# Performance work log

Hardware: AMD Instinct MI355X
Metric: run time of the kernel (lower is better)

## Reference

```python
import jax, jax.numpy as jnp
import numpy as np

B, T, K, H = 2, 2048, 1024, 16


def setup_inputs() -> dict:
    key = jax.random.key(0)
    ks = jax.random.split(key, 9)
    sc = 0.02
    return {
        "x": jax.random.normal(ks[0], (B, T, K), dtype=jnp.float32),
        "Wq_w": jax.random.normal(ks[1], (K, K), dtype=jnp.float32) * sc,
        "Wq_b": jax.random.normal(ks[2], (K,), dtype=jnp.float32) * sc,
        "Wk_w": jax.random.normal(ks[3], (K, K), dtype=jnp.float32) * sc,
        "Wk_b": jax.random.normal(ks[4], (K,), dtype=jnp.float32) * sc,
        "Wv_w": jax.random.normal(ks[5], (K, K), dtype=jnp.float32) * sc,
        "Wv_b": jax.random.normal(ks[6], (K,), dtype=jnp.float32) * sc,
        "Wo_w": jax.random.normal(ks[7], (K, K), dtype=jnp.float32) * sc,
        "Wo_b": jax.random.normal(ks[8], (K,), dtype=jnp.float32) * sc,
    }


def reference(x, Wq_w, Wq_b, Wk_w, Wk_b, Wv_w, Wv_b, Wo_w, Wo_b):
    b, t, k = x.shape
    h = H
    s = k // h
    # nn.Linear: y = x @ W^T + b
    q = x @ Wq_w.T + Wq_b
    kk = x @ Wk_w.T + Wk_b
    v = x @ Wv_w.T + Wv_b
    # [b, t, h, s] -> [b, h, t, s]
    q = q.reshape(b, t, h, s).transpose(0, 2, 1, 3)
    kk = kk.reshape(b, t, h, s).transpose(0, 2, 1, 3)
    v = v.reshape(b, t, h, s).transpose(0, 2, 1, 3)
    # scores [b, h, t, t]
    dot = jnp.einsum("bhqd,bhkd->bhqk", q, kk)
    # causal mask: upper triangle (offset=1) set to -inf BEFORE scaling
    causal = jnp.tril(jnp.ones((t, t), dtype=bool))
    dot = jnp.where(causal, dot, -jnp.inf)
    # NOTE: original scales by sqrt(k) (full model dim), not sqrt(head_dim)
    dot = dot / jnp.sqrt(jnp.asarray(k, dot.dtype))
    attn = jax.nn.softmax(dot, axis=-1)
    out = jnp.einsum("bhqk,bhkd->bhqd", attn, v)  # [b, h, t, s]
    out = out.transpose(0, 2, 1, 3).reshape(b, t, k)
    return out @ Wo_w.T + Wo_b
```

## Files before the change

### kernel.cpp

```cpp
#include <hip/hip_runtime.h>

typedef unsigned short u16;
typedef unsigned int u32;
typedef __bf16 bf16x8 __attribute__((ext_vector_type(8)));
typedef float f32x4 __attribute__((ext_vector_type(4)));
typedef unsigned short u16x8 __attribute__((ext_vector_type(8)));
typedef unsigned int u32x4 __attribute__((ext_vector_type(4)));

#define B_ 2
#define T_ 2048
#define K_ 1024
#define H_ 16
#define S_ 64
#define MKC 4194304
#define QSCALE 0.04508422f

__device__ __forceinline__ u16 f2bf(float f) {
  unsigned int u = __builtin_bit_cast(unsigned int, f);
  u += 0x7fffu + ((u >> 16) & 1u);
  return (u16)(u >> 16);
}

__device__ __forceinline__ f32x4 MFMA(bf16x8 a, bf16x8 b, f32x4 c) {
  return __builtin_amdgcn_mfma_f32_16x16x32_bf16(a, b, c, 0, 0, 0);
}

__device__ __forceinline__ void gld16(const void* g, void* l) {
  __builtin_amdgcn_global_load_lds((const __attribute__((address_space(1))) void*)g,
                                   (__attribute__((address_space(3))) void*)l, 16, 0, 0);
}

template <int N>
__device__ __forceinline__ void waitv() {
  asm volatile("s_waitcnt vmcnt(%0)" ::"i"(N) : "memory");
}
__device__ __forceinline__ void memfence_barrier() {
  asm volatile("" ::: "memory");
  __builtin_amdgcn_s_barrier();
}

__global__ __launch_bounds__(256) void cvt_all(const float* __restrict__ x,
                                               const float* __restrict__ W0,
                                               const float* __restrict__ W1,
                                               const float* __restrict__ W2,
                                               const float* __restrict__ W3,
                                               u16* __restrict__ xb,
                                               u16* __restrict__ wb) {
  const int i = blockIdx.x * 256 + threadIdx.x;
  const float* src;
  u16* dst;
  if (i < 524288) {
    src = x + (size_t)i * 8;
    dst = xb + (size_t)i * 8;
  } else {
    const int j = i - 524288;
    const int sel = j >> 17;
    const float* W = sel == 0 ? W0 : sel == 1 ? W1 : sel == 2 ? W2 : W3;
    src = W + (size_t)(j & 131071) * 8;
    dst = wb + (size_t)j * 8;
  }
  const float4* s = (const float4*)src;
  float4 f0 = s[0], f1 = s[1];
  u16x8 p;
  p[0] = f2bf(f0.x); p[1] = f2bf(f0.y); p[2] = f2bf(f0.z); p[3] = f2bf(f0.w);
  p[4] = f2bf(f1.x); p[5] = f2bf(f1.y); p[6] = f2bf(f1.z); p[7] = f2bf(f1.w);
  *(u16x8*)dst = p;
}

template <int OMODE, int BN>
__global__ __launch_bounds__(256) void gemm16(const u16* __restrict__ A,
                                              const u16* __restrict__ Bm,
                                              const float* __restrict__ b0,
                                              const float* __restrict__ b1,
                                              const float* __restrict__ b2,
                                              void* __restrict__ C0,
                                              int M, int N, int K) {
  constexpr int NF = BN / 32;
  constexpr int SOPS = 2 + BN / 64;
  __shared__ u16 As[2][128 * 32];
  __shared__ u16 Bs[2][BN * 32];
  const int bm = blockIdx.x * 128;
  const int bn = blockIdx.y * BN;
  const int tid = threadIdx.x;
  const int w = tid >> 6, lane = tid & 63;
  const int wr = (w >> 1) * 64, wc = (w & 1) * (BN / 2);
  const int lr = lane & 15, g = lane >> 4;
  const int lk = g * 8;
  const int srow = lane >> 2, scol = (lane & 3) * 8;

  f32x4 acc[4][NF] = {};

  auto stg = [&](int buf, int k0) {
#pragma unroll
    for (int i = 0; i < 2; ++i) {
      const int rbase = (i * 4 + w) * 16;
      gld16(A + (size_t)(bm + rbase + srow) * K + k0 + scol, &As[buf][rbase * 32]);
    }
#pragma unroll
    for (int i = 0; i < BN / 64; ++i) {
      const int rbase = (i * 4 + w) * 16;
      gld16(Bm + (size_t)(bn + rbase + srow) * K + k0 + scol, &Bs[buf][rbase * 32]);
    }
  };

  stg(0, 0);
  const int NK = K >> 5;
  for (int kk = 0; kk < NK; ++kk) {
    const int buf = kk & 1;
    const bool pf = (kk + 1 < NK);
    if (pf) {
      stg(buf ^ 1, (kk + 1) * 32);
      waitv<SOPS>();
    } else {
      waitv<0>();
    }
    __builtin_amdgcn_s_barrier();
    bf16x8 af[4], bfr[NF];
#pragma unroll
    for (int m = 0; m < 4; ++m)
      af[m] = *(const bf16x8*)&As[buf][(wr + m * 16 + lr) * 32 + lk];
#pragma unroll
    for (int n = 0; n < NF; ++n)
      bfr[n] = *(const bf16x8*)&Bs[buf][(wc + n * 16 + lr) * 32 + lk];
#pragma unroll
    for (int m = 0; m < 4; ++m)
#pragma unroll
      for (int n = 0; n < NF; ++n)
        acc[m][n] = MFMA(af[m], bfr[n], acc[m][n]);
    memfence_barrier();
  }

  const int sel = (OMODE == 2) ? 0 : (bn >> 10);
  const float* bp = (OMODE == 2) ? b0 : (sel == 0 ? b0 : sel == 1 ? b1 : b2);
#pragma unroll
  for (int n = 0; n < NF; ++n) {
    const int col = bn + wc + n * 16 + lr;
    const float bv = bp[(OMODE == 2) ? col : (col & 1023)];
#pragma unroll
    for (int m = 0; m < 4; ++m) {
#pragma unroll
      for (int r = 0; r < 4; ++r) {
        const int row = bm + wr + m * 16 + g * 4 + r;
        float v = acc[m][n][r] + bv;
        if (OMODE == 2) {
          ((float*)C0)[(size_t)row * N + col] = v;
        } else {
          u16* dst = (u16*)C0;
          const int cc = col & 1023;
          if (sel == 2) {
            const int bb = row >> 11, t = row & 2047, hh = cc >> 6, ss = cc & 63;
            dst[(size_t)2 * MKC + (((size_t)(bb * H_ + hh) * S_ + ss) << 11) + t] = f2bf(v);
          } else {
            if (sel == 0) v *= QSCALE;
            dst[(size_t)sel * MKC + (size_t)row * 1024 + cc] = f2bf(v);
          }
        }
      }
    }
  }
}

__global__ __launch_bounds__(256) void attn_fwd(const u16* __restrict__ Q,
                                                const u16* __restrict__ Kb,
                                                const u16* __restrict__ Vt,
                                                u16* __restrict__ O) {
  __shared__ u16 Ks[2][64 * 64];
  __shared__ u16 Vs[2][64 * 64];
  const int tid = threadIdx.x;
  const int w = tid >> 6, lane = tid & 63;
  const int qh = lane & 15;
  const int g = lane >> 4;
  const int bh = blockIdx.x;
  const int b = bh >> 4, h = bh & 15;
  const int yy = blockIdx.y, t7 = yy & 7, kq = yy >> 3;
  const int qtile = (kq == 0) ? (31 - t7) : (kq == 1) ? (16 + t7)
                   : (kq == 2) ? (15 - t7) : t7;
  const int qb = qtile * 64;
  const int qw = qb + w * 16;
  const int myq = qw + qh;

  const size_t qoff = (size_t)(b * T_ + qw + qh) * K_ + h * S_ + g * 8;
  const bf16x8 bq0 = *(const bf16x8*)(Q + qoff);
  const bf16x8 bq1 = *(const bf16x8*)(Q + qoff + 32);

  const int srow = lane >> 3;
  const int sl8 = ((lane & 7) ^ srow) * 8;
  int kvp[2];
#pragma unroll
  for (int i = 0; i < 2; ++i) {
    const int rho = w * 16 + i * 8 + srow;
    const int a = rho >> 4;
    kvp[i] = ((a >> 1) << 5) | (((rho >> 2) & 3) << 3) | ((a & 1) << 2) | (rho & 3);
  }
  auto stage = [&](int buf, int k0) {
#pragma unroll
    for (int i = 0; i < 2; ++i) {
      const int rb = w * 16 + i * 8;
      gld16(Kb + (size_t)(b * T_ + k0 + kvp[i]) * K_ + h * S_ + sl8,
            &Ks[buf][rb * 64]);
    }
#pragma unroll
    for (int i = 0; i < 2; ++i) {
      const int rb = w * 16 + i * 8;
      gld16(Vt + (size_t)(bh * S_ + rb + srow) * T_ + k0 + sl8,
            &Vs[buf][rb * 64]);
    }
  };

  const int nk = qtile + 1;
  stage(0, 0);

  float m = -INFINITY, lsum = 0.f;
  f32x4 o[4] = {};
  const int ksw = qh & 7;

  for (int kt = 0; kt < nk; ++kt) {
    const int k0 = kt * 64;
    const int cur = kt & 1;
    const bool pf = (kt + 1 < nk);
    if (pf) {
      stage(cur ^ 1, k0 + 64);
      waitv<4>();
    } else {
      waitv<0>();
    }
    __builtin_amdgcn_s_barrier();

    f32x4 s[4];
    __builtin_amdgcn_s_setprio(1);
#pragma unroll
    for (int a = 0; a < 4; ++a) {
      const u16* kr = &Ks[cur][(a * 16 + qh) * 64];
      const bf16x8 kf0 = *(const bf16x8*)(kr + ((g ^ ksw) * 8));
      const bf16x8 kf1 = *(const bf16x8*)(kr + (((4 + g) ^ ksw) * 8));
      f32x4 z = {0.f, 0.f, 0.f, 0.f};
      z = MFMA(kf0, bq0, z);
      s[a] = MFMA(kf1, bq1, z);
    }
    __builtin_amdgcn_s_setprio(0);

    float p[4][4];
    float vmax = -INFINITY;
    if (k0 + 63 > qw) {
#pragma unroll
      for (int a = 0; a < 4; ++a)
#pragma unroll
        for (int r = 0; r < 4; ++r) {
          const int kv = k0 + ((a >> 1) << 5) + (g << 3) + ((a & 1) << 2) + r;
          p[a][r] = (kv <= myq) ? s[a][r] : -INFINITY;
          vmax = fmaxf(vmax, p[a][r]);
        }
    } else {
#pragma unroll
      for (int a = 0; a < 4; ++a)
#pragma unroll
        for (int r = 0; r < 4; ++r) {
          p[a][r] = s[a][r];
          vmax = fmaxf(vmax, p[a][r]);
        }
    }
    vmax = fmaxf(vmax, __shfl_xor(vmax, 16));
    vmax = fmaxf(vmax, __shfl_xor(vmax, 32));

    if (__any(vmax > m + 11.5f)) {
      const float mnew = fmaxf(m, vmax);
      const float alpha = __builtin_amdgcn_exp2f(m - mnew);
      m = mnew;
      lsum *= alpha;
      float aR[4];
#pragma unroll
      for (int r = 0; r < 4; ++r) aR[r] = __shfl(alpha, 4 * g + r);
#pragma unroll
      for (int n = 0; n < 4; ++n)
#pragma unroll
        for (int r = 0; r < 4; ++r) o[n][r] *= aR[r];
    }

    float ls = 0.f;
#pragma unroll
    for (int a = 0; a < 4; ++a)
#pragma unroll
      for (int r = 0; r < 4; ++r) {
        p[a][r] = __builtin_amdgcn_exp2f(p[a][r] - m);
        ls += p[a][r];
      }
    ls += __shfl_xor(ls, 16);
    ls += __shfl_xor(ls, 32);
    lsum += ls;

    __builtin_amdgcn_s_setprio(1);
#pragma unroll
    for (int c = 0; c < 2; ++c) {
      u32 t0, t1, t2, t3;
      asm("v_cvt_pk_bf16_f32 %0, %1, %2" : "=v"(t0) : "v"(p[2 * c][0]), "v"(p[2 * c][1]));
      asm("v_cvt_pk_bf16_f32 %0, %1, %2" : "=v"(t1) : "v"(p[2 * c][2]), "v"(p[2 * c][3]));
      asm("v_cvt_pk_bf16_f32 %0, %1, %2" : "=v"(t2) : "v"(p[2 * c + 1][0]), "v"(p[2 * c + 1][1]));
      asm("v_cvt_pk_bf16_f32 %0, %1, %2" : "=v"(t3) : "v"(p[2 * c + 1][2]), "v"(p[2 * c + 1][3]));
      u32x4 tv; tv[0] = t0; tv[1] = t1; tv[2] = t2; tv[3] = t3;
      const bf16x8 pa = __builtin_bit_cast(bf16x8, tv);
#pragma unroll
      for (int n = 0; n < 4; ++n) {
        const bf16x8 vf =
            *(const bf16x8*)(&Vs[cur][(16 * n + qh) * 64] + (((c * 4 + g) ^ ksw) * 8));
        o[n] = MFMA(pa, vf, o[n]);
      }
    }
    __builtin_amdgcn_s_setprio(0);

    memfence_barrier();
  }

  const float inv = 1.f / lsum;
  float iR[4];
#pragma unroll
  for (int r = 0; r < 4; ++r) iR[r] = __shfl(inv, 4 * g + r);
#pragma unroll
  for (int r = 0; r < 4; ++r) {
    const size_t row = (size_t)(b * T_ + qw + 4 * g + r);
#pragma unroll
    for (int n = 0; n < 4; ++n)
      O[row * K_ + h * S_ + n * 16 + qh] = f2bf(o[n][r] * iR[r]);
  }
}

extern "C" void kernel_launch(void* const* d_in, const int* in_sizes, int n_in,
                              void* d_out, int out_size, void* d_ws, size_t ws_size,
                              hipStream_t stream) {
  (void)in_sizes; (void)n_in; (void)out_size; (void)ws_size;
  const float* x  = (const float*)d_in[0];
  const float* Wq = (const float*)d_in[1];
  const float* bq = (const float*)d_in[2];
  const float* Wk = (const float*)d_in[3];
  const float* bk = (const float*)d_in[4];
  const float* Wv = (const float*)d_in[5];
  const float* bv = (const float*)d_in[6];
  const float* Wo = (const float*)d_in[7];
  const float* bo = (const float*)d_in[8];
  float* out = (float*)d_out;

  const size_t MK = (size_t)MKC;
  const size_t WK = (size_t)K_ * K_;
  u16* Qb  = (u16*)d_ws;
  u16* Kbf = Qb + MK;
  u16* Vtb = Kbf + MK;
  u16* AO  = Vtb + MK;
  u16* xb  = AO + MK;
  u16* Wqkv = xb + MK;
  u16* Wob  = Wqkv + 3 * WK;

  dim3 blk(256);
  cvt_all<<<dim3(4096), blk, 0, stream>>>(x, Wq, Wk, Wv, Wo, xb, Wqkv);
  gemm16<3, 128><<<dim3(32, 24), blk, 0, stream>>>(xb, Wqkv, bq, bk, bv, Qb,
                                                   B_ * T_, 3 * K_, K_);
  attn_fwd<<<dim3(B_ * H_, T_ / 64), blk, 0, stream>>>(Qb, Kbf, Vtb, AO);
  gemm16<2, 64><<<dim3(32, 16), blk, 0, stream>>>(AO, Wob, bo, bo, bo, out,
                                                  B_ * T_, K_, K_);
}
```

Measured before the change: 110.9 us.

## Rewrite attention as single-wave blocks with register-prefetched K/V and no LDS

The attention kernel moves from 256-thread blocks that stage K/V tiles through double-buffered shared memory with barriers to 64-thread single-wave blocks. Each block handles 32 queries as two 16-row tiles and reads K and V fragments straight from global memory into registers, with ping-pong register prefetch of the next tile. Block indices are remapped so each XCD gets a fixed set of heads, and the per-step lsum shuffle reduction is deferred to the end. This removes LDS traffic and barriers, but K/V is no longer shared across waves, so global/L2 reads rise and register pressure goes up. The old heavy-tiles-first ordering is also dropped.

```diff
diff --git a/kernel.cpp b/kernel.cpp
--- a/kernel.cpp
+++ b/kernel.cpp
@@ -160,166 +160,168 @@
   }
 }
 
-__global__ __launch_bounds__(256) void attn_fwd(const u16* __restrict__ Q,
-                                                const u16* __restrict__ Kb,
-                                                const u16* __restrict__ Vt,
-                                                u16* __restrict__ O) {
-  __shared__ u16 Ks[2][64 * 64];
-  __shared__ u16 Vs[2][64 * 64];
-  const int tid = threadIdx.x;
-  const int w = tid >> 6, lane = tid & 63;
+__global__ __launch_bounds__(64) void attn_fwd(const u16* __restrict__ Q,
+                                               const u16* __restrict__ Kb,
+                                               const u16* __restrict__ Vt,
+                                               u16* __restrict__ O) {
+  const int lane = threadIdx.x;
   const int qh = lane & 15;
   const int g = lane >> 4;
-  const int bh = blockIdx.x;
+  const int n = blockIdx.x;
+  const int xcd = n & 7, slot = n >> 3;
+  const int bh = xcd * 4 + (slot & 3);
+  const int qidx = slot >> 2;
   const int b = bh >> 4, h = bh & 15;
-  const int yy = blockIdx.y, t7 = yy & 7, kq = yy >> 3;
-  const int qtile = (kq == 0) ? (31 - t7) : (kq == 1) ? (16 + t7)
-                   : (kq == 2) ? (15 - t7) : t7;
-  const int qb = qtile * 64;
-  const int qw = qb + w * 16;
-  const int myq = qw + qh;
-
-  const size_t qoff = (size_t)(b * T_ + qw + qh) * K_ + h * S_ + g * 8;
-  const bf16x8 bq0 = *(const bf16x8*)(Q + qoff);
-  const bf16x8 bq1 = *(const bf16x8*)(Q + qoff + 32);
-
-  const int srow = lane >> 3;
-  const int sl8 = ((lane & 7) ^ srow) * 8;
-  int kvp[2];
-#pragma unroll
-  for (int i = 0; i < 2; ++i) {
-    const int rho = w * 16 + i * 8 + srow;
-    const int a = rho >> 4;
-    kvp[i] = ((a >> 1) << 5) | (((rho >> 2) & 3) << 3) | ((a & 1) << 2) | (rho & 3);
-  }
-  auto stage = [&](int buf, int k0) {
-#pragma unroll
-    for (int i = 0; i < 2; ++i) {
-      const int rb = w * 16 + i * 8;
-      gld16(Kb + (size_t)(b * T_ + k0 + kvp[i]) * K_ + h * S_ + sl8,
-            &Ks[buf][rb * 64]);
-    }
-#pragma unroll
-    for (int i = 0; i < 2; ++i) {
-      const int rb = w * 16 + i * 8;
-      gld16(Vt + (size_t)(bh * S_ + rb + srow) * T_ + k0 + sl8,
-            &Vs[buf][rb * 64]);
+  const int qb = qidx * 32;
+  const int nk = (qidx >> 1) + 1;
+
+  bf16x8 bq[2][2];
+#pragma unroll
+  for (int j = 0; j < 2; ++j) {
+    const size_t qoff = (size_t)(b * T_ + qb + j * 16 + qh) * K_ + h * S_ + g * 8;
+    bq[j][0] = *(const bf16x8*)(Q + qoff);
+    bq[j][1] = *(const bf16x8*)(Q + qoff + 32);
+  }
+
+  const int kvb = ((qh >> 2) << 3) | (qh & 3);
+  const u16* kbase = Kb + (size_t)(b * T_ + kvb) * K_ + h * S_ + g * 8;
+  const u16* vbase = Vt + ((size_t)bh * S_ + qh) * T_ + g * 8;
+
+  auto loadK = [&](auto& kf, int k0) {
+#pragma unroll
+    for (int a = 0; a < 4; ++a) {
+      const u16* kp = kbase + (size_t)(k0 + ((a >> 1) << 5) + ((a & 1) << 2)) * K_;
+      kf[a][0] = *(const bf16x8*)kp;
+      kf[a][1] = *(const bf16x8*)(kp + 32);
     }
   };
-
-  const int nk = qtile + 1;
-  stage(0, 0);
-
-  float m = -INFINITY, lsum = 0.f;
-  f32x4 o[4] = {};
-  const int ksw = qh & 7;
-
-  for (int kt = 0; kt < nk; ++kt) {
+  auto loadV = [&](auto& vf, int k0) {
+#pragma unroll
+    for (int c = 0; c < 2; ++c)
+#pragma unroll
+      for (int nn = 0; nn < 4; ++nn)
+        vf[c][nn] = *(const bf16x8*)(vbase + (size_t)(nn * 16) * T_ + k0 + c * 32);
+  };
+
+  float m[2], lsum[2];
+  f32x4 o[2][4] = {};
+#pragma unroll
+  for (int j = 0; j < 2; ++j) { m[j] = -INFINITY; lsum[j] = 0.f; }
+
+  bf16x8 kfA[4][2], kfB[4][2], vfA[2][4], vfB[2][4];
+  loadK(kfA, 0);
+  loadV(vfA, 0);
+
+  auto step = [&](auto& kf, auto& vf, auto& kfN, auto& vfN, int kt, bool pf) {
     const int k0 = kt * 64;
-    const int cur = kt & 1;
-    const bool pf = (kt + 1 < nk);
-    if (pf) {
-      stage(cur ^ 1, k0 + 64);
-      waitv<4>();
-    } else {
-      waitv<0>();
-    }
-    __builtin_amdgcn_s_barrier();
-
-    f32x4 s[4];
+    f32x4 s[2][4];
     __builtin_amdgcn_s_setprio(1);
 #pragma unroll
-    for (int a = 0; a < 4; ++a) {
-      const u16* kr = &Ks[cur][(a * 16 + qh) * 64];
-      const bf16x8 kf0 = *(const bf16x8*)(kr + ((g ^ ksw) * 8));
-      const bf16x8 kf1 = *(const bf16x8*)(kr + (((4 + g) ^ ksw) * 8));
-      f32x4 z = {0.f, 0.f, 0.f, 0.f};
-      z = MFMA(kf0, bq0, z);
-      s[a] = MFMA(kf1, bq1, z);
-    }
+    for (int j = 0; j < 2; ++j)
+#pragma unroll
+      for (int a = 0; a < 4; ++a) {
+        f32x4 z = {0.f, 0.f, 0.f, 0.f};
+        z = MFMA(kf[a][0], bq[j][0], z);
+        s[j][a] = MFMA(kf[a][1], bq[j][1], z);
+      }
     __builtin_amdgcn_s_setprio(0);
-
-    float p[4][4];
-    float vmax = -INFINITY;
-    if (k0 + 63 > qw) {
+    if (pf) loadK(kfN, k0 + 64);
+
+    float p[2][4][4];
+#pragma unroll
+    for (int j = 0; j < 2; ++j) {
+      const int qw = qb + 16 * j;
+      const int myq = qw + qh;
+      float vmax = -INFINITY;
+      if (k0 + 63 > qw) {
+#pragma unroll
+        for (int a = 0; a < 4; ++a)
+#pragma unroll
+          for (int r = 0; r < 4; ++r) {
+            const int kv = k0 + ((a >> 1) << 5) + (g << 3) + ((a & 1) << 2) + r;
+            p[j][a][r] = (kv <= myq) ? s[j][a][r] : -INFINITY;
+            vmax = fmaxf(vmax, p[j][a][r]);
+          }
+      } else {
+#pragma unroll
+        for (int a = 0; a < 4; ++a)
+#pragma unroll
+          for (int r = 0; r < 4; ++r) {
+            p[j][a][r] = s[j][a][r];
+            vmax = fmaxf(vmax, p[j][a][r]);
+          }
+      }
+      vmax = fmaxf(vmax, __shfl_xor(vmax, 16));
+      vmax = fmaxf(vmax, __shfl_xor(vmax, 32));
+
+      if (__any(vmax > m[j] + 11.5f)) {
+        const float mnew = fmaxf(m[j], vmax);
+        const float alpha = __builtin_amdgcn_exp2f(m[j] - mnew);
+        m[j] = mnew;
+        lsum[j] *= alpha;
+        float aR[4];
+#pragma unroll
+        for (int r = 0; r < 4; ++r) aR[r] = __shfl(alpha, 4 * g + r);
+#pragma unroll
+        for (int nn = 0; nn < 4; ++nn)
+#pragma unroll
+          for (int r = 0; r < 4; ++r) o[j][nn][r] *= aR[r];
+      }
+
+      float ls = 0.f;
 #pragma unroll
       for (int a = 0; a < 4; ++a)
 #pragma unroll
         for (int r = 0; r < 4; ++r) {
-          const int kv = k0 + ((a >> 1) << 5) + (g << 3) + ((a & 1) << 2) + r;
-          p[a][r] = (kv <= myq) ? s[a][r] : -INFINITY;
-          vmax = fmaxf(vmax, p[a][r]);
+          p[j][a][r] = __builtin_amdgcn_exp2f(p[j][a][r] - m[j]);
+          ls += p[j][a][r];
         }
-    } else {
-#pragma unroll
-      for (int a = 0; a < 4; ++a)
-#pragma unroll
-        for (int r = 0; r < 4; ++r) {
-          p[a][r] = s[a][r];
-          vmax = fmaxf(vmax, p[a][r]);
-        }
-    }
-    vmax = fmaxf(vmax, __shfl_xor(vmax, 16));
-    vmax = fmaxf(vmax, __shfl_xor(vmax, 32));
-
-    if (__any(vmax > m + 11.5f)) {
-      const float mnew = fmaxf(m, vmax);
-      const float alpha = __builtin_amdgcn_exp2f(m - mnew);
-      m = mnew;
-      lsum *= alpha;
-      float aR[4];
-#pragma unroll
-      for (int r = 0; r < 4; ++r) aR[r] = __shfl(alpha, 4 * g + r);
-#pragma unroll
-      for (int n = 0; n < 4; ++n)
-#pragma unroll
-        for (int r = 0; r < 4; ++r) o[n][r] *= aR[r];
-    }
-
-    float ls = 0.f;
-#pragma unroll
-    for (int a = 0; a < 4; ++a)
-#pragma unroll
-      for (int r = 0; r < 4; ++r) {
-        p[a][r] = __builtin_amdgcn_exp2f(p[a][r] - m);
-        ls += p[a][r];
-      }
-    ls += __shfl_xor(ls, 16);
-    ls += __shfl_xor(ls, 32);
-    lsum += ls;
+      lsum[j] += ls;
+    }
 
     __builtin_amdgcn_s_setprio(1);
 #pragma unroll
-    for (int c = 0; c < 2; ++c) {
-      u32 t0, t1, t2, t3;
-      asm("v_cvt_pk_bf16_f32 %0, %1, %2" : "=v"(t0) : "v"(p[2 * c][0]), "v"(p[2 * c][1]));
-      asm("v_cvt_pk_bf16_f32 %0, %1, %2" : "=v"(t1) : "v"(p[2 * c][2]), "v"(p[2 * c][3]));
-      asm("v_cvt_pk_bf16_f32 %0, %1, %2" : "=v"(t2) : "v"(p[2 * c + 1][0]), "v"(p[2 * c + 1][1]));
-      asm("v_cvt_pk_bf16_f32 %0, %1, %2" : "=v"(t3) : "v"(p[2 * c + 1][2]), "v"(p[2 * c + 1][3]));
-      u32x4 tv; tv[0] = t0; tv[1] = t1; tv[2] = t2; tv[3] = t3;
-      const bf16x8 pa = __builtin_bit_cast(bf16x8, tv);
-#pragma unroll
-      for (int n = 0; n < 4; ++n) {
-        const bf16x8 vf =
-            *(const bf16x8*)(&Vs[cur][(16 * n + qh) * 64] + (((c * 4 + g) ^ ksw) * 8));
-        o[n] = MFMA(pa, vf, o[n]);
-      }
-    }
+    for (int j = 0; j < 2; ++j)
+#pragma unroll
+      for (int c = 0; c < 2; ++c) {
+        u32 t0, t1, t2, t3;
+        asm("v_cvt_pk_bf16_f32 %0, %1, %2" : "=v"(t0) : "v"(p[j][2 * c][0]), "v"(p[j][2 * c][1]));
+        asm("v_cvt_pk_bf16_f32 %0, %1, %2" : "=v"(t1) : "v"(p[j][2 * c][2]), "v"(p[j][2 * c][3]));
+        asm("v_cvt_pk_bf16_f32 %0, %1, %2" : "=v"(t2) : "v"(p[j][2 * c + 1][0]), "v"(p[j][2 * c + 1][1]));
+        asm("v_cvt_pk_bf16_f32 %0, %1, %2" : "=v"(t3) : "v"(p[j][2 * c + 1][2]), "v"(p[j][2 * c + 1][3]));
+        u32x4 tv; tv[0] = t0; tv[1] = t1; tv[2] = t2; tv[3] = t3;
+        const bf16x8 pa = __builtin_bit_cast(bf16x8, tv);
+#pragma unroll
+        for (int nn = 0; nn < 4; ++nn)
+          o[j][nn] = MFMA(pa, vf[c][nn], o[j][nn]);
+      }
     __builtin_amdgcn_s_setprio(0);
-
-    memfence_barrier();
-  }
-
-  const float inv = 1.f / lsum;
-  float iR[4];
-#pragma unroll
-  for (int r = 0; r < 4; ++r) iR[r] = __shfl(inv, 4 * g + r);
-#pragma unroll
-  for (int r = 0; r < 4; ++r) {
-    const size_t row = (size_t)(b * T_ + qw + 4 * g + r);
-#pragma unroll
-    for (int n = 0; n < 4; ++n)
-      O[row * K_ + h * S_ + n * 16 + qh] = f2bf(o[n][r] * iR[r]);
+    if (pf) loadV(vfN, k0 + 64);
+  };
+
+  int kt = 0;
+  while (true) {
+    { const bool pf = kt + 1 < nk; step(kfA, vfA, kfB, vfB, kt, pf); if (!pf) break; }
+    ++kt;
+    { const bool pf = kt + 1 < nk; step(kfB, vfB, kfA, vfA, kt, pf); if (!pf) break; }
+    ++kt;
+  }
+
+#pragma unroll
+  for (int j = 0; j < 2; ++j) {
+    lsum[j] += __shfl_xor(lsum[j], 16);
+    lsum[j] += __shfl_xor(lsum[j], 32);
+    const float inv = 1.f / lsum[j];
+    float iR[4];
+#pragma unroll
+    for (int r = 0; r < 4; ++r) iR[r] = __shfl(inv, 4 * g + r);
+#pragma unroll
+    for (int r = 0; r < 4; ++r) {
+      const size_t row = (size_t)(b * T_ + qb + 16 * j + 4 * g + r);
+#pragma unroll
+      for (int nn = 0; nn < 4; ++nn)
+        O[row * K_ + h * S_ + nn * 16 + qh] = f2bf(o[j][nn][r] * iR[r]);
+    }
   }
 }
 
@@ -352,7 +354,7 @@
   cvt_all<<<dim3(4096), blk, 0, stream>>>(x, Wq, Wk, Wv, Wo, xb, Wqkv);
   gemm16<3, 128><<<dim3(32, 24), blk, 0, stream>>>(xb, Wqkv, bq, bk, bv, Qb,
                                                    B_ * T_, 3 * K_, K_);
-  attn_fwd<<<dim3(B_ * H_, T_ / 64), blk, 0, stream>>>(Qb, Kbf, Vtb, AO);
+  attn_fwd<<<dim3(2048), dim3(64), 0, stream>>>(Qb, Kbf, Vtb, AO);
   gemm16<2, 64><<<dim3(32, 16), blk, 0, stream>>>(AO, Wob, bo, bo, bo, out,
                                                   B_ * T_, K_, K_);
 }
```

New measurement: 141.1 us. 27.2% more time.

## Compute softmax row sums via MFMA with ones vector, simplify mask and max

Applied to the files above, without the earlier changes.

The row-sum of softmax probabilities now comes from an extra MFMA against a bf16 ones operand that accumulates alongside the output, replacing per-lane adds plus cross-lane shuffles. The final normalization reads the sum directly from the accumulator layout, so the shuffle of the inverse is gone. The change also precomputes K/V staging pointers that advance by increments, simplifies the causal-mask comparison to a per-thread threshold, and restructures the max reduction into 3-input max calls. The cost is one extra MFMA per chunk, and the sum is now taken over bf16-rounded probabilities, which slightly changes numerics.

```diff
diff --git a/kernel.cpp b/kernel.cpp
--- a/kernel.cpp
+++ b/kernel.cpp
@@ -37,6 +37,9 @@
 __device__ __forceinline__ void memfence_barrier() {
   asm volatile("" ::: "memory");
   __builtin_amdgcn_s_barrier();
+}
+__device__ __forceinline__ float fmax3(float a, float b, float c) {
+  return fmaxf(fmaxf(a, b), c);
 }
 
 __global__ __launch_bounds__(256) void cvt_all(const float* __restrict__ x,
@@ -192,34 +195,36 @@
     const int a = rho >> 4;
     kvp[i] = ((a >> 1) << 5) | (((rho >> 2) & 3) << 3) | ((a & 1) << 2) | (rho & 3);
   }
-  auto stage = [&](int buf, int k0) {
-#pragma unroll
-    for (int i = 0; i < 2; ++i) {
-      const int rb = w * 16 + i * 8;
-      gld16(Kb + (size_t)(b * T_ + k0 + kvp[i]) * K_ + h * S_ + sl8,
-            &Ks[buf][rb * 64]);
-    }
-#pragma unroll
-    for (int i = 0; i < 2; ++i) {
-      const int rb = w * 16 + i * 8;
-      gld16(Vt + (size_t)(bh * S_ + rb + srow) * T_ + k0 + sl8,
-            &Vs[buf][rb * 64]);
-    }
+  const u16* kq0 = Kb + (size_t)(b * T_ + kvp[0]) * K_ + h * S_ + sl8;
+  const u16* kq1 = Kb + (size_t)(b * T_ + kvp[1]) * K_ + h * S_ + sl8;
+  const u16* vq0 = Vt + (size_t)(bh * S_ + w * 16 + srow) * T_ + sl8;
+  const u16* vq1 = Vt + (size_t)(bh * S_ + w * 16 + 8 + srow) * T_ + sl8;
+  auto stage = [&](int buf) {
+    gld16(kq0, &Ks[buf][(w * 16) * 64]);
+    gld16(kq1, &Ks[buf][(w * 16 + 8) * 64]);
+    gld16(vq0, &Vs[buf][(w * 16) * 64]);
+    gld16(vq1, &Vs[buf][(w * 16 + 8) * 64]);
+    kq0 += 64 * K_; kq1 += 64 * K_; vq0 += 64; vq1 += 64;
   };
 
   const int nk = qtile + 1;
-  stage(0, 0);
-
-  float m = -INFINITY, lsum = 0.f;
+  stage(0);
+
+  float m = -INFINITY;
   f32x4 o[4] = {};
+  f32x4 o_l = {};
   const int ksw = qh & 7;
+  u16x8 ov;
+#pragma unroll
+  for (int i = 0; i < 8; ++i) ov[i] = 0x3F80;
+  const bf16x8 ones = __builtin_bit_cast(bf16x8, ov);
 
   for (int kt = 0; kt < nk; ++kt) {
     const int k0 = kt * 64;
     const int cur = kt & 1;
     const bool pf = (kt + 1 < nk);
     if (pf) {
-      stage(cur ^ 1, k0 + 64);
+      stage(cur ^ 1);
       waitv<4>();
     } else {
       waitv<0>();
@@ -240,25 +245,27 @@
     __builtin_amdgcn_s_setprio(0);
 
     float p[4][4];
-    float vmax = -INFINITY;
     if (k0 + 63 > qw) {
+      const int thr = myq - k0 - (g << 3);
 #pragma unroll
       for (int a = 0; a < 4; ++a)
 #pragma unroll
         for (int r = 0; r < 4; ++r) {
-          const int kv = k0 + ((a >> 1) << 5) + (g << 3) + ((a & 1) << 2) + r;
-          p[a][r] = (kv <= myq) ? s[a][r] : -INFINITY;
-          vmax = fmaxf(vmax, p[a][r]);
+          const int C = ((a >> 1) << 5) + ((a & 1) << 2) + r;
+          p[a][r] = (C <= thr) ? s[a][r] : -INFINITY;
         }
     } else {
 #pragma unroll
       for (int a = 0; a < 4; ++a)
 #pragma unroll
-        for (int r = 0; r < 4; ++r) {
-          p[a][r] = s[a][r];
-          vmax = fmaxf(vmax, p[a][r]);
-        }
-    }
+        for (int r = 0; r < 4; ++r) p[a][r] = s[a][r];
+    }
+    float x0 = fmax3(p[0][0], p[0][1], p[0][2]);
+    float x1 = fmax3(p[0][3], p[1][0], p[1][1]);
+    float x2 = fmax3(p[1][2], p[1][3], p[2][0]);
+    float x3 = fmax3(p[2][1], p[2][2], p[2][3]);
+    float x4 = fmax3(p[3][0], p[3][1], p[3][2]);
+    float vmax = fmax3(fmax3(x0, x1, x2), x3, fmaxf(x4, p[3][3]));
     vmax = fmaxf(vmax, __shfl_xor(vmax, 16));
     vmax = fmaxf(vmax, __shfl_xor(vmax, 32));
 
@@ -266,27 +273,22 @@
       const float mnew = fmaxf(m, vmax);
       const float alpha = __builtin_amdgcn_exp2f(m - mnew);
       m = mnew;
-      lsum *= alpha;
       float aR[4];
 #pragma unroll
       for (int r = 0; r < 4; ++r) aR[r] = __shfl(alpha, 4 * g + r);
 #pragma unroll
-      for (int n = 0; n < 4; ++n)
-#pragma unroll
-        for (int r = 0; r < 4; ++r) o[n][r] *= aR[r];
-    }
-
-    float ls = 0.f;
+      for (int nn = 0; nn < 4; ++nn)
+#pragma unroll
+        for (int r = 0; r < 4; ++r) o[nn][r] *= aR[r];
+#pragma unroll
+      for (int r = 0; r < 4; ++r) o_l[r] *= aR[r];
+    }
+
 #pragma unroll
     for (int a = 0; a < 4; ++a)
 #pragma unroll
-      for (int r = 0; r < 4; ++r) {
+      for (int r = 0; r < 4; ++r)
         p[a][r] = __builtin_amdgcn_exp2f(p[a][r] - m);
-        ls += p[a][r];
-      }
-    ls += __shfl_xor(ls, 16);
-    ls += __shfl_xor(ls, 32);
-    lsum += ls;
 
     __builtin_amdgcn_s_setprio(1);
 #pragma unroll
@@ -298,11 +300,12 @@
       asm("v_cvt_pk_bf16_f32 %0, %1, %2" : "=v"(t3) : "v"(p[2 * c + 1][2]), "v"(p[2 * c + 1][3]));
       u32x4 tv; tv[0] = t0; tv[1] = t1; tv[2] = t2; tv[3] = t3;
       const bf16x8 pa = __builtin_bit_cast(bf16x8, tv);
-#pragma unroll
-      for (int n = 0; n < 4; ++n) {
+      o_l = MFMA(pa, ones, o_l);
+#pragma unroll
+      for (int nn = 0; nn < 4; ++nn) {
         const bf16x8 vf =
-            *(const bf16x8*)(&Vs[cur][(16 * n + qh) * 64] + (((c * 4 + g) ^ ksw) * 8));
-        o[n] = MFMA(pa, vf, o[n]);
+            *(const bf16x8*)(&Vs[cur][(16 * nn + qh) * 64] + (((c * 4 + g) ^ ksw) * 8));
+        o[nn] = MFMA(pa, vf, o[nn]);
       }
     }
     __builtin_amdgcn_s_setprio(0);
@@ -310,16 +313,13 @@
     memfence_barrier();
   }
 
-  const float inv = 1.f / lsum;
-  float iR[4];
-#pragma unroll
-  for (int r = 0; r < 4; ++r) iR[r] = __shfl(inv, 4 * g + r);
 #pragma unroll
   for (int r = 0; r < 4; ++r) {
+    const float inv = 1.f / o_l[r];
     const size_t row = (size_t)(b * T_ + qw + 4 * g + r);
 #pragma unroll
-    for (int n = 0; n < 4; ++n)
-      O[row * K_ + h * S_ + n * 16 + qh] = f2bf(o[n][r] * iR[r]);
+    for (int nn = 0; nn < 4; ++nn)
+      O[row * K_ + h * S_ + nn * 16 + qh] = f2bf(o[nn][r] * inv);
   }
 }
 
```

Result: no change. 109.7 us (-1.1%).
